# Optimization experiments

Hardware: AMD Instinct MI355X
Metric: run time of the kernel (lower is better)

Reference implementation:

```python
import jax, jax.numpy as jnp
import numpy as np

N_NODES, FEAT, EMB, BATCH, NUM_SAMPLE = 100000, 256, 256, 10000, 32


def setup_inputs() -> dict:
    key = jax.random.key(0)
    ks = jax.random.split(key, 8)
    sc = 1.0 / np.sqrt(FEAT).astype(np.float32)
    return {
        "nodes": jax.random.randint(ks[0], (BATCH,), 0, N_NODES),
        "neigh_idx": jax.random.randint(ks[1], (BATCH, NUM_SAMPLE), 0, N_NODES),
        "id2feat": jax.random.normal(ks[2], (N_NODES, FEAT), jnp.float32),
        "Wq": jax.random.normal(ks[3], (FEAT, EMB), jnp.float32) * sc,
        "bq": jnp.zeros((EMB,), jnp.float32),
        "Wk": jax.random.normal(ks[4], (FEAT, EMB), jnp.float32) * sc,
        "bk": jnp.zeros((EMB,), jnp.float32),
        "Wv": jax.random.normal(ks[5], (FEAT, EMB), jnp.float32) * sc,
        "bv": jnp.zeros((EMB,), jnp.float32),
    }


def reference(nodes, neigh_idx, id2feat, Wq, bq, Wk, bk, Wv, bv):
    # Gather: self feats [B, F] and sampled neighbor feats [B, S, F]
    self_feats = id2feat[nodes]
    neigh_feats = id2feat[neigh_idx]
    S = neigh_idx.shape[1]
    # Keys/values over [neighbors, self] -> [B, S+1, F]
    cat = jnp.concatenate([neigh_feats, self_feats[:, None, :]], axis=1)
    Q = self_feats @ Wq + bq               # [B, E]
    K = cat @ Wk + bk                       # [B, S+1, E]
    V = cat @ Wv + bv                       # [B, S+1, E]
    scores = jnp.einsum('be,bse->bs', Q, K)  # [B, S+1]
    # Faithful to original mask loop: with full neighbor lists, columns >= num_sample
    # (the appended self key) are masked out.
    mask = jnp.arange(S + 1) >= S
    scores = jnp.where(mask[None, :], -jnp.inf, scores)
    attn = jax.nn.softmax(scores, axis=-1)   # [B, S+1]
    return jnp.einsum('bs,bse->be', attn, V)  # [B, E]
```

## Files before the change

### kernel.cpp

```cpp
#include <hip/hip_runtime.h>
#include <math.h>

#define F 256
#define E 256
#define S 32
#define CH 4

__global__ __launch_bounds__(256) void prep_M(const float* __restrict__ Wq,
                                              const float* __restrict__ bq,
                                              const float* __restrict__ Wk,
                                              float* __restrict__ M,
                                              float* __restrict__ c) {
    const int i = blockIdx.x;
    const int j = threadIdx.x;
    __shared__ float row[E];
    row[j] = (i < F) ? Wq[i * E + j] : bq[j];
    __syncthreads();
    float acc = 0.f;
#pragma unroll 8
    for (int e = 0; e < E; e += 4) {
        float4 w = *reinterpret_cast<const float4*>(&Wk[j * E + e]);
        acc += row[e] * w.x + row[e + 1] * w.y + row[e + 2] * w.z + row[e + 3] * w.w;
    }
    if (i < F) M[i * F + j] = acc;
    else       c[j] = acc;
}

__global__ __launch_bounds__(256) void gemm_bias(const float* __restrict__ X,
                                                 const int* __restrict__ idx,
                                                 const float* __restrict__ W,
                                                 const float* __restrict__ bias,
                                                 float* __restrict__ out,
                                                 int rows) {
    __shared__ float xsT[64][68];
    __shared__ float wt[64][64];
    const int tid = threadIdx.x;
    const int tx = tid & 15, ty = tid >> 4;
    const int bn = blockIdx.x, bm = blockIdx.y;
    const int jb = bn * 64 + tx * 4;
    float acc[4][4] = {{0.f}};

    for (int k0 = 0; k0 < F; k0 += 64) {
#pragma unroll
        for (int p = 0; p < 4; ++p) {
            const int lr = p * 16 + ty;
            const int lk = tx * 4;
            const int gr = bm * 64 + lr;
            const int grc = gr < rows ? gr : rows - 1;
            const long grow = idx ? (long)idx[grc] : (long)grc;
            float4 v = *reinterpret_cast<const float4*>(&X[grow * F + k0 + lk]);
            xsT[lk + 0][lr] = v.x; xsT[lk + 1][lr] = v.y;
            xsT[lk + 2][lr] = v.z; xsT[lk + 3][lr] = v.w;
            const int wk = p * 16 + ty;
            float4 wv = *reinterpret_cast<const float4*>(&W[(size_t)(k0 + wk) * E + bn * 64 + tx * 4]);
            *reinterpret_cast<float4*>(&wt[wk][tx * 4]) = wv;
        }
        __syncthreads();
#pragma unroll 16
        for (int k = 0; k < 64; ++k) {
            float4 a = *reinterpret_cast<const float4*>(&xsT[k][ty * 4]);
            float4 b = *reinterpret_cast<const float4*>(&wt[k][tx * 4]);
            acc[0][0] += a.x * b.x; acc[0][1] += a.x * b.y; acc[0][2] += a.x * b.z; acc[0][3] += a.x * b.w;
            acc[1][0] += a.y * b.x; acc[1][1] += a.y * b.y; acc[1][2] += a.y * b.z; acc[1][3] += a.y * b.w;
            acc[2][0] += a.z * b.x; acc[2][1] += a.z * b.y; acc[2][2] += a.z * b.z; acc[2][3] += a.z * b.w;
            acc[3][0] += a.w * b.x; acc[3][1] += a.w * b.y; acc[3][2] += a.w * b.z; acc[3][3] += a.w * b.w;
        }
        __syncthreads();
    }

    const float4 bb = *reinterpret_cast<const float4*>(&bias[jb]);
#pragma unroll
    for (int v = 0; v < 4; ++v) {
        const int r = bm * 64 + ty * 4 + v;
        if (r < rows) {
            float4 o;
            o.x = acc[v][0] + bb.x; o.y = acc[v][1] + bb.y;
            o.z = acc[v][2] + bb.z; o.w = acc[v][3] + bb.w;
            *reinterpret_cast<float4*>(&out[(size_t)r * E + jb]) = o;
        }
    }
}

__device__ __forceinline__ void ld_chunk(float4* d, int idxv, int s0,
                                         const float* __restrict__ t, int lane) {
#pragma unroll
    for (int j = 0; j < CH; ++j) {
        const int nid = __builtin_amdgcn_readlane(idxv, s0 + j);
        d[j] = *reinterpret_cast<const float4*>(&t[(size_t)nid * F + lane * 4]);
    }
}

__device__ __forceinline__ void proc_chunk(const float4* v, const float4 qv,
                                           float& m, float& l, float4& acc) {
#pragma unroll
    for (int j = 0; j < CH; ++j) {
        float p = v[j].x * qv.x + v[j].y * qv.y + v[j].z * qv.z + v[j].w * qv.w;
#pragma unroll
        for (int off = 32; off; off >>= 1) p += __shfl_xor(p, off);
        if (p <= m) {
            const float w = __expf(p - m);
            l += w;
            acc.x += w * v[j].x; acc.y += w * v[j].y;
            acc.z += w * v[j].z; acc.w += w * v[j].w;
        } else {
            const float c = __expf(m - p);
            l = l * c + 1.f;
            acc.x = acc.x * c + v[j].x; acc.y = acc.y * c + v[j].y;
            acc.z = acc.z * c + v[j].z; acc.w = acc.w * c + v[j].w;
            m = p;
        }
    }
}

__global__ __launch_bounds__(256) void attn_gather(const int* __restrict__ neigh_idx,
                                                   const float* __restrict__ id2feat,
                                                   float* __restrict__ qtm,
                                                   int B) {
    const int node = blockIdx.x * 4 + (threadIdx.x >> 6);
    const int lane = threadIdx.x & 63;
    if (node >= B) return;

    const int idxv = neigh_idx[node * S + (lane & (S - 1))];
    const float4 qv = *reinterpret_cast<const float4*>(&qtm[(size_t)node * F + lane * 4]);

    float m = -INFINITY, l = 0.f;
    float4 acc = make_float4(0.f, 0.f, 0.f, 0.f);

    float4 va[CH], vb[CH];
    ld_chunk(va, idxv, 0, id2feat, lane);
    ld_chunk(vb, idxv, 4, id2feat, lane);
    proc_chunk(va, qv, m, l, acc);
    ld_chunk(va, idxv, 8, id2feat, lane);
    proc_chunk(vb, qv, m, l, acc);
    ld_chunk(vb, idxv, 12, id2feat, lane);
    proc_chunk(va, qv, m, l, acc);
    ld_chunk(va, idxv, 16, id2feat, lane);
    proc_chunk(vb, qv, m, l, acc);
    ld_chunk(vb, idxv, 20, id2feat, lane);
    proc_chunk(va, qv, m, l, acc);
    ld_chunk(va, idxv, 24, id2feat, lane);
    proc_chunk(vb, qv, m, l, acc);
    ld_chunk(vb, idxv, 28, id2feat, lane);
    proc_chunk(va, qv, m, l, acc);
    proc_chunk(vb, qv, m, l, acc);

    const float inv = 1.0f / l;
    float4 o;
    o.x = acc.x * inv; o.y = acc.y * inv; o.z = acc.z * inv; o.w = acc.w * inv;
    *reinterpret_cast<float4*>(&qtm[(size_t)node * F + lane * 4]) = o;
}

extern "C" void kernel_launch(void* const* d_in, const int* in_sizes, int n_in,
                              void* d_out, int out_size, void* d_ws, size_t ws_size,
                              hipStream_t stream) {
    const int*   nodes   = (const int*)d_in[0];
    const int*   neigh   = (const int*)d_in[1];
    const float* id2feat = (const float*)d_in[2];
    const float* Wq      = (const float*)d_in[3];
    const float* bq      = (const float*)d_in[4];
    const float* Wk      = (const float*)d_in[5];
    const float* Wv      = (const float*)d_in[7];
    const float* bv      = (const float*)d_in[8];
    float* out = (float*)d_out;
    const int B = in_sizes[0];

    float* Mbuf = (float*)d_ws;
    float* cbuf = Mbuf + F * F;
    float* qtm  = cbuf + F;

    prep_M<<<dim3(F + 1), dim3(256), 0, stream>>>(Wq, bq, Wk, Mbuf, cbuf);
    gemm_bias<<<dim3(4, (B + 63) / 64), dim3(256), 0, stream>>>(id2feat, nodes, Mbuf, cbuf, qtm, B);
    attn_gather<<<dim3((B + 3) / 4), dim3(256), 0, stream>>>(neigh, id2feat, qtm, B);
    gemm_bias<<<dim3(4, (B + 63) / 64), dim3(256), 0, stream>>>(qtm, nullptr, Wv, bv, out, B);
}
```

Before: 134.7 us.

## Replace FP32 SIMT GEMMs with split-bf16 MFMA GEMMs and fused weight prep

The two FP32 register-tiled GEMMs (gathered self-features times M, and attention output times Wv) become MFMA bf16 GEMMs. Each operand is split into hi and lo bf16 parts and three MFMAs (hh, hl, lh) are accumulated to keep roughly FP32 accuracy. A single prep kernel builds the transposed, split M and Wv matrices plus the bias vector c, and each GEMM block now covers all 256 output columns for 64 rows. This removes the scalar FMA bottleneck, at the cost of three times the matrix-core work, extra conversion ALU, and somewhat lower precision than true FP32.

```diff
diff --git a/kernel.cpp b/kernel.cpp
--- a/kernel.cpp
+++ b/kernel.cpp
@@ -5,78 +5,157 @@
 #define E 256
 #define S 32
 #define CH 4
-
-__global__ __launch_bounds__(256) void prep_M(const float* __restrict__ Wq,
-                                              const float* __restrict__ bq,
-                                              const float* __restrict__ Wk,
-                                              float* __restrict__ M,
-                                              float* __restrict__ c) {
-    const int i = blockIdx.x;
-    const int j = threadIdx.x;
-    __shared__ float row[E];
-    row[j] = (i < F) ? Wq[i * E + j] : bq[j];
-    __syncthreads();
-    float acc = 0.f;
+#define LDK 40
+
+typedef __attribute__((ext_vector_type(8))) short short8;
+typedef __attribute__((ext_vector_type(4))) float f32x4;
+
+__device__ __forceinline__ ushort f2bf(float x) {
+    uint u = __float_as_uint(x);
+    uint r = (u + 0x7fffu + ((u >> 16) & 1u)) >> 16;
+    return (ushort)r;
+}
+__device__ __forceinline__ float bf2f(ushort h) {
+    return __uint_as_float(((uint)h) << 16);
+}
+
+__global__ __launch_bounds__(256) void prep_all(const float* __restrict__ Wq,
+                                                const float* __restrict__ bq,
+                                                const float* __restrict__ Wk,
+                                                const float* __restrict__ Wv,
+                                                ushort* __restrict__ MT_hi,
+                                                ushort* __restrict__ MT_lo,
+                                                ushort* __restrict__ WvT_hi,
+                                                ushort* __restrict__ WvT_lo,
+                                                float* __restrict__ c) {
+    const int t = threadIdx.x;
+    if (blockIdx.x < 256) {
+        const int j = blockIdx.x;
+        __shared__ float wkj[F];
+        wkj[t] = Wk[j * F + t];
+        __syncthreads();
+        float acc = 0.f;
 #pragma unroll 8
-    for (int e = 0; e < E; e += 4) {
-        float4 w = *reinterpret_cast<const float4*>(&Wk[j * E + e]);
-        acc += row[e] * w.x + row[e + 1] * w.y + row[e + 2] * w.z + row[e + 3] * w.w;
-    }
-    if (i < F) M[i * F + j] = acc;
-    else       c[j] = acc;
-}
-
-__global__ __launch_bounds__(256) void gemm_bias(const float* __restrict__ X,
+        for (int e = 0; e < F; e += 4) {
+            float4 wq = *reinterpret_cast<const float4*>(&Wq[t * E + e]);
+            acc += wkj[e] * wq.x + wkj[e + 1] * wq.y + wkj[e + 2] * wq.z + wkj[e + 3] * wq.w;
+        }
+        const ushort hi = f2bf(acc);
+        MT_hi[j * F + t] = hi;
+        MT_lo[j * F + t] = f2bf(acc - bf2f(hi));
+        if (t == 0) {
+            float s = 0.f;
+            for (int e = 0; e < F; ++e) s += wkj[e] * bq[e];
+            c[j] = s;
+        }
+    } else {
+        const int j = blockIdx.x - 256;
+        const float v = Wv[t * E + j];
+        const ushort hi = f2bf(v);
+        WvT_hi[j * F + t] = hi;
+        WvT_lo[j * F + t] = f2bf(v - bf2f(hi));
+    }
+}
+
+__global__ __launch_bounds__(256) void mfma_gemm(const float* __restrict__ X,
                                                  const int* __restrict__ idx,
-                                                 const float* __restrict__ W,
+                                                 const ushort* __restrict__ BTh,
+                                                 const ushort* __restrict__ BTl,
                                                  const float* __restrict__ bias,
                                                  float* __restrict__ out,
                                                  int rows) {
-    __shared__ float xsT[64][68];
-    __shared__ float wt[64][64];
+    __shared__ ushort Ah[64][LDK], Al[64][LDK];
+    __shared__ ushort Bh[256][LDK], Bl[256][LDK];
+
     const int tid = threadIdx.x;
-    const int tx = tid & 15, ty = tid >> 4;
-    const int bn = blockIdx.x, bm = blockIdx.y;
-    const int jb = bn * 64 + tx * 4;
-    float acc[4][4] = {{0.f}};
-
-    for (int k0 = 0; k0 < F; k0 += 64) {
-#pragma unroll
-        for (int p = 0; p < 4; ++p) {
-            const int lr = p * 16 + ty;
-            const int lk = tx * 4;
-            const int gr = bm * 64 + lr;
-            const int grc = gr < rows ? gr : rows - 1;
-            const long grow = idx ? (long)idx[grc] : (long)grc;
-            float4 v = *reinterpret_cast<const float4*>(&X[grow * F + k0 + lk]);
-            xsT[lk + 0][lr] = v.x; xsT[lk + 1][lr] = v.y;
-            xsT[lk + 2][lr] = v.z; xsT[lk + 3][lr] = v.w;
-            const int wk = p * 16 + ty;
-            float4 wv = *reinterpret_cast<const float4*>(&W[(size_t)(k0 + wk) * E + bn * 64 + tx * 4]);
-            *reinterpret_cast<float4*>(&wt[wk][tx * 4]) = wv;
-        }
+    const int lane = tid & 63, wave = tid >> 6;
+    const int wm = wave >> 1, wn = wave & 1;
+    const int fr = lane & 15, fk = lane >> 4;
+    const int row0 = blockIdx.x * 64;
+
+    const int arL = tid >> 2;
+    const int akL = (tid & 3) * 8;
+    const int ar = row0 + arL;
+    const int arc = ar < rows ? ar : rows - 1;
+    const long arow = idx ? (long)idx[arc] : (long)arc;
+    const float* aptr = X + arow * (long)F + akL;
+
+    const ushort* bhp = BTh + (size_t)tid * F;
+    const ushort* blp = BTl + (size_t)tid * F;
+
+    f32x4 acc[2][8];
+#pragma unroll
+    for (int m = 0; m < 2; ++m)
+#pragma unroll
+        for (int n = 0; n < 8; ++n) acc[m][n] = (f32x4){0.f, 0.f, 0.f, 0.f};
+
+    for (int k0 = 0; k0 < F; k0 += 32) {
+        const float4 v0 = *reinterpret_cast<const float4*>(&aptr[k0]);
+        const float4 v1 = *reinterpret_cast<const float4*>(&aptr[k0 + 4]);
+        const uint4 bh0 = *reinterpret_cast<const uint4*>(&bhp[k0]);
+        const uint4 bh1 = *reinterpret_cast<const uint4*>(&bhp[k0 + 8]);
+        const uint4 bh2 = *reinterpret_cast<const uint4*>(&bhp[k0 + 16]);
+        const uint4 bh3 = *reinterpret_cast<const uint4*>(&bhp[k0 + 24]);
+        const uint4 bl0 = *reinterpret_cast<const uint4*>(&blp[k0]);
+        const uint4 bl1 = *reinterpret_cast<const uint4*>(&blp[k0 + 8]);
+        const uint4 bl2 = *reinterpret_cast<const uint4*>(&blp[k0 + 16]);
+        const uint4 bl3 = *reinterpret_cast<const uint4*>(&blp[k0 + 24]);
+
+        const float xv[8] = {v0.x, v0.y, v0.z, v0.w, v1.x, v1.y, v1.z, v1.w};
+        ushort h[8], l[8];
+#pragma unroll
+        for (int jj = 0; jj < 8; ++jj) {
+            h[jj] = f2bf(xv[jj]);
+            l[jj] = f2bf(xv[jj] - bf2f(h[jj]));
+        }
+        uint4 ph, pl;
+        ph.x = (uint)h[0] | ((uint)h[1] << 16); ph.y = (uint)h[2] | ((uint)h[3] << 16);
+        ph.z = (uint)h[4] | ((uint)h[5] << 16); ph.w = (uint)h[6] | ((uint)h[7] << 16);
+        pl.x = (uint)l[0] | ((uint)l[1] << 16); pl.y = (uint)l[2] | ((uint)l[3] << 16);
+        pl.z = (uint)l[4] | ((uint)l[5] << 16); pl.w = (uint)l[6] | ((uint)l[7] << 16);
+
         __syncthreads();
-#pragma unroll 16
-        for (int k = 0; k < 64; ++k) {
-            float4 a = *reinterpret_cast<const float4*>(&xsT[k][ty * 4]);
-            float4 b = *reinterpret_cast<const float4*>(&wt[k][tx * 4]);
-            acc[0][0] += a.x * b.x; acc[0][1] += a.x * b.y; acc[0][2] += a.x * b.z; acc[0][3] += a.x * b.w;
-            acc[1][0] += a.y * b.x; acc[1][1] += a.y * b.y; acc[1][2] += a.y * b.z; acc[1][3] += a.y * b.w;
-            acc[2][0] += a.z * b.x; acc[2][1] += a.z * b.y; acc[2][2] += a.z * b.z; acc[2][3] += a.z * b.w;
-            acc[3][0] += a.w * b.x; acc[3][1] += a.w * b.y; acc[3][2] += a.w * b.z; acc[3][3] += a.w * b.w;
-        }
+        *reinterpret_cast<uint4*>(&Ah[arL][akL]) = ph;
+        *reinterpret_cast<uint4*>(&Al[arL][akL]) = pl;
+        *reinterpret_cast<uint4*>(&Bh[tid][0])  = bh0;
+        *reinterpret_cast<uint4*>(&Bh[tid][8])  = bh1;
+        *reinterpret_cast<uint4*>(&Bh[tid][16]) = bh2;
+        *reinterpret_cast<uint4*>(&Bh[tid][24]) = bh3;
+        *reinterpret_cast<uint4*>(&Bl[tid][0])  = bl0;
+        *reinterpret_cast<uint4*>(&Bl[tid][8])  = bl1;
+        *reinterpret_cast<uint4*>(&Bl[tid][16]) = bl2;
+        *reinterpret_cast<uint4*>(&Bl[tid][24]) = bl3;
         __syncthreads();
-    }
-
-    const float4 bb = *reinterpret_cast<const float4*>(&bias[jb]);
-#pragma unroll
-    for (int v = 0; v < 4; ++v) {
-        const int r = bm * 64 + ty * 4 + v;
-        if (r < rows) {
-            float4 o;
-            o.x = acc[v][0] + bb.x; o.y = acc[v][1] + bb.y;
-            o.z = acc[v][2] + bb.z; o.w = acc[v][3] + bb.w;
-            *reinterpret_cast<float4*>(&out[(size_t)r * E + jb]) = o;
+
+        const short8 a_h0 = *reinterpret_cast<const short8*>(&Ah[wm * 32 + fr][fk * 8]);
+        const short8 a_l0 = *reinterpret_cast<const short8*>(&Al[wm * 32 + fr][fk * 8]);
+        const short8 a_h1 = *reinterpret_cast<const short8*>(&Ah[wm * 32 + 16 + fr][fk * 8]);
+        const short8 a_l1 = *reinterpret_cast<const short8*>(&Al[wm * 32 + 16 + fr][fk * 8]);
+#pragma unroll
+        for (int n = 0; n < 8; ++n) {
+            const short8 b_h = *reinterpret_cast<const short8*>(&Bh[wn * 128 + n * 16 + fr][fk * 8]);
+            const short8 b_l = *reinterpret_cast<const short8*>(&Bl[wn * 128 + n * 16 + fr][fk * 8]);
+            acc[0][n] = __builtin_amdgcn_mfma_f32_16x16x32_bf16(a_h0, b_h, acc[0][n], 0, 0, 0);
+            acc[0][n] = __builtin_amdgcn_mfma_f32_16x16x32_bf16(a_h0, b_l, acc[0][n], 0, 0, 0);
+            acc[0][n] = __builtin_amdgcn_mfma_f32_16x16x32_bf16(a_l0, b_h, acc[0][n], 0, 0, 0);
+            acc[1][n] = __builtin_amdgcn_mfma_f32_16x16x32_bf16(a_h1, b_h, acc[1][n], 0, 0, 0);
+            acc[1][n] = __builtin_amdgcn_mfma_f32_16x16x32_bf16(a_h1, b_l, acc[1][n], 0, 0, 0);
+            acc[1][n] = __builtin_amdgcn_mfma_f32_16x16x32_bf16(a_l1, b_h, acc[1][n], 0, 0, 0);
+        }
+    }
+
+#pragma unroll
+    for (int n = 0; n < 8; ++n) {
+        const int col = wn * 128 + n * 16 + fr;
+        const float bb = bias[col];
+#pragma unroll
+        for (int m = 0; m < 2; ++m) {
+#pragma unroll
+            for (int r = 0; r < 4; ++r) {
+                const int orow = row0 + wm * 32 + m * 16 + fk * 4 + r;
+                if (orow < rows)
+                    out[(size_t)orow * E + col] = acc[m][n][r] + bb;
+            }
         }
     }
 }
@@ -164,12 +243,18 @@
     float* out = (float*)d_out;
     const int B = in_sizes[0];
 
-    float* Mbuf = (float*)d_ws;
-    float* cbuf = Mbuf + F * F;
-    float* qtm  = cbuf + F;
-
-    prep_M<<<dim3(F + 1), dim3(256), 0, stream>>>(Wq, bq, Wk, Mbuf, cbuf);
-    gemm_bias<<<dim3(4, (B + 63) / 64), dim3(256), 0, stream>>>(id2feat, nodes, Mbuf, cbuf, qtm, B);
+    ushort* MT_hi  = (ushort*)d_ws;
+    ushort* MT_lo  = MT_hi + 65536;
+    ushort* WvT_hi = MT_lo + 65536;
+    ushort* WvT_lo = WvT_hi + 65536;
+    float*  cbuf   = (float*)(WvT_lo + 65536);
+    float*  qtm    = cbuf + 256;
+
+    prep_all<<<dim3(512), dim3(256), 0, stream>>>(Wq, bq, Wk, Wv,
+                                                  MT_hi, MT_lo, WvT_hi, WvT_lo, cbuf);
+    mfma_gemm<<<dim3((B + 63) / 64), dim3(256), 0, stream>>>(id2feat, nodes,
+                                                             MT_hi, MT_lo, cbuf, qtm, B);
     attn_gather<<<dim3((B + 3) / 4), dim3(256), 0, stream>>>(neigh, id2feat, qtm, B);
-    gemm_bias<<<dim3(4, (B + 63) / 64), dim3(256), 0, stream>>>(qtm, nullptr, Wv, bv, out, B);
-}
+    mfma_gemm<<<dim3((B + 63) / 64), dim3(256), 0, stream>>>(qtm, nullptr,
+                                                             WvT_hi, WvT_lo, bv, out, B);
+}
```

Measured after the change: 122.5 us. -9.0%, faster.
